# Optimization experiments

Hardware: AMD Instinct MI355X
Metric: run time of the kernel (lower is better)

The kernel has to match this reference:

```python
import jax, jax.numpy as jnp
import numpy as np

H = 16  # num heads
ROPE_BASE = 10000.0

def _rope(t):
    # t: [B, T, H, D]; half-split (rotate_half / LLaMA-style) rotary embedding
    B, T, nH, D = t.shape
    half = D // 2
    inv_freq = 1.0 / (ROPE_BASE ** (jnp.arange(0, half, dtype=jnp.float32) / half))
    ang = jnp.arange(T, dtype=jnp.float32)[:, None] * inv_freq[None, :]  # [T, half]
    cos = jnp.cos(ang)[None, :, None, :]  # [1,T,1,half]
    sin = jnp.sin(ang)[None, :, None, :]
    t1, t2 = t[..., :half], t[..., half:]
    return jnp.concatenate([t1 * cos - t2 * sin, t2 * cos + t1 * sin], axis=-1)

def setup_inputs() -> dict:
    key = jax.random.key(0)
    ks = jax.random.split(key, 5)
    B, T, C = 2, 2048, 1024
    s = 1.0 / np.sqrt(C)
    return {
        "x": jax.random.normal(ks[0], (B, T, C), jnp.float32),
        "Wqkv": jax.random.normal(ks[1], (C, 3 * C), jnp.float32) * s,
        "bqkv": jnp.zeros((3 * C,), jnp.float32),
        "Wout": jax.random.normal(ks[2], (C, C), jnp.float32) * s,
        "bout": jnp.zeros((C,), jnp.float32),
    }

def reference(x, Wqkv, bqkv, Wout, bout):
    B, T, C = x.shape
    D = C // H
    qkv = (x @ Wqkv + bqkv).reshape(B, T, 3, H, D)
    q, k, v = qkv[:, :, 0], qkv[:, :, 1], qkv[:, :, 2]  # [B,T,H,D]
    q = _rope(q)
    k = _rope(k)
    scale = 1.0 / jnp.sqrt(jnp.asarray(D, x.dtype))
    scores = jnp.einsum('bqhd,bkhd->bhqk', q, k) * scale
    probs = jax.nn.softmax(scores, axis=-1)
    attn = jnp.einsum('bhqk,bkhd->bqhd', probs, v).reshape(B, T, C)
    return attn @ Wout + bout
```

## Files before the change

kernel.cpp:

```cpp
#include <hip/hip_runtime.h>

typedef float f32x4 __attribute__((ext_vector_type(4)));
typedef short bf16x8 __attribute__((ext_vector_type(8)));
typedef short bf16x4 __attribute__((ext_vector_type(4)));

#define DEV __device__ __forceinline__

DEV unsigned short f2bf(float x) {
  union { float f; unsigned u; } v; v.f = x;
  unsigned r = v.u + 0x7fffu + ((v.u >> 16) & 1u);
  return (unsigned short)(r >> 16);
}
DEV float bf2f(unsigned short h) {
  union { unsigned u; float f; } v; v.u = ((unsigned)h) << 16;
  return v.f;
}

#if defined(__has_builtin)
# if __has_builtin(__builtin_amdgcn_global_load_lds)
#  define HAVE_GLL 1
# endif
# if __has_builtin(__builtin_amdgcn_exp2f)
#  define EXP2(x) __builtin_amdgcn_exp2f(x)
# else
#  define EXP2(x) exp2f(x)
# endif
#else
# define EXP2(x) exp2f(x)
#endif

DEV unsigned pk_bf16_trunc(float a, float b) {
  return __builtin_amdgcn_perm(__float_as_uint(b), __float_as_uint(a), 0x07060302u);
}
DEV unsigned pk_bf16_rnd(float a, float b) {
  return ((unsigned)f2bf(b) << 16) | f2bf(a);
}

DEV void g2l16(const unsigned short* g, unsigned short* l) {
#ifdef HAVE_GLL
  __builtin_amdgcn_global_load_lds((const __attribute__((address_space(1))) void*)g,
                                   (__attribute__((address_space(3))) void*)l, 16, 0, 0);
#else
  *(uint4*)l = *(const uint4*)g;
#endif
}

DEV f32x4 mfma16x16x16(bf16x4 a, bf16x4 b, f32x4 c) {
#if defined(__has_builtin) && __has_builtin(__builtin_amdgcn_mfma_f32_16x16x16bf16_1k)
  return __builtin_amdgcn_mfma_f32_16x16x16bf16_1k(a, b, c, 0, 0, 0);
#else
  asm volatile("v_mfma_f32_16x16x16_bf16 %0, %1, %2, %0" : "+v"(c) : "v"(a), "v"(b));
  return c;
#endif
}

__global__ __launch_bounds__(256) void prep(const float* __restrict__ x,
                                            const float* __restrict__ Wqkv,
                                            const float* __restrict__ Wout,
                                            float* cosb, float* sinb,
                                            unsigned short* __restrict__ A1,
                                            unsigned short* __restrict__ W1t,
                                            unsigned short* __restrict__ W2t) {
  __shared__ float t[64 * 65];
  int blk = blockIdx.x;
  if (blk < 256) {
    int i = blk * 256 + threadIdx.x;
    int tt = i >> 5, d = i & 31;
    float invf = (float)(1.0 / pow(10000.0, (double)d / 32.0));
    float ang = (float)tt * invf;
    cosb[i] = (float)cos((double)ang);
    sinb[i] = (float)sin((double)ang);
    return;
  }
  if (blk < 4352) {
    int i = (blk - 256) * 256 + threadIdx.x;
    f32x4 v = ((const f32x4*)x)[i];
    ushort4 o;
    o.x = f2bf(v[0]); o.y = f2bf(v[1]); o.z = f2bf(v[2]); o.w = f2bf(v[3]);
    ((ushort4*)A1)[i] = o;
    return;
  }
  const float* W; unsigned short* Wt; int N, bidx;
  if (blk < 5120) { W = Wqkv; Wt = W1t; N = 3072; bidx = blk - 4352; }
  else            { W = Wout; Wt = W2t; N = 1024; bidx = blk - 5120; }
  int k0 = (bidx & 15) * 64, n0 = (bidx >> 4) * 64;
  for (int idx = threadIdx.x; idx < 4096; idx += 256) {
    int kl = idx >> 6, nl = idx & 63;
    t[kl * 65 + nl] = W[(size_t)(k0 + kl) * N + n0 + nl];
  }
  __syncthreads();
  for (int idx = threadIdx.x; idx < 4096; idx += 256) {
    int nl = idx >> 6, kl = idx & 63;
    Wt[(size_t)(n0 + nl) * 1024 + k0 + kl] = f2bf(t[kl * 65 + nl]);
  }
}

#define QSCALE 0.180336880f
__global__ __launch_bounds__(256, 2) void gemm_qkv(
    const unsigned short* __restrict__ A, const unsigned short* __restrict__ Bt,
    const float* __restrict__ bias, const float* __restrict__ cosb,
    const float* __restrict__ sinb, unsigned short* __restrict__ QK,
    unsigned short* __restrict__ Vt) {
  const int K = 1024;
  __shared__ alignas(16) unsigned short As[128 * 64];
  __shared__ alignas(16) unsigned short Bs[128 * 64];
  const int tid = threadIdx.x;
  const int lane = tid & 63, wave = tid >> 6;
  const int l15 = lane & 15, quad = lane >> 4;
  const int m0 = blockIdx.y * 128, n0 = blockIdx.x * 128;
  const int wm = (wave & 1) * 64, wn = (wave >> 1) * 64;

  f32x4 acc[4][4];
#pragma unroll
  for (int i = 0; i < 4; i++)
#pragma unroll
    for (int j = 0; j < 4; j++)
#pragma unroll
      for (int r = 0; r < 4; r++) acc[i][j][r] = 0.f;

  for (int kt = 0; kt < 16; ++kt) {
    __syncthreads();
#pragma unroll
    for (int i = 0; i < 4; ++i) {
      int u = i * 256 + tid;
      int row = u >> 3;
      int kcg = (u & 7) ^ (row & 7);
      g2l16(A  + (size_t)(m0 + row) * K + (kt << 6) + (kcg << 3), As + u * 8);
      g2l16(Bt + (size_t)(n0 + row) * K + (kt << 6) + (kcg << 3), Bs + u * 8);
    }
    __syncthreads();
#pragma unroll
    for (int ks = 0; ks < 2; ++ks) {
      const int kc = ks * 4 + quad;
      bf16x8 af[4], bfr[4];
#pragma unroll
      for (int t = 0; t < 4; ++t) {
        int mrow = wm + t * 16 + l15;
        af[t] = *(const bf16x8*)(As + (mrow * 8 + (kc ^ (mrow & 7))) * 8);
        int nrow = wn + t * 16 + l15;
        bfr[t] = *(const bf16x8*)(Bs + (nrow * 8 + (kc ^ (nrow & 7))) * 8);
      }
#pragma unroll
      for (int mt = 0; mt < 4; ++mt)
#pragma unroll
        for (int nt = 0; nt < 4; ++nt)
          acc[mt][nt] = __builtin_amdgcn_mfma_f32_16x16x32_bf16(af[mt], bfr[nt], acc[mt][nt], 0, 0, 0);
    }
  }
  const int headcol = n0 + wn;
  const int b = m0 >> 11;
  float bb[4];
#pragma unroll
  for (int nt = 0; nt < 4; ++nt) bb[nt] = bias[headcol + nt * 16 + l15];

  if (headcol < 2048) {
    const float scale = (headcol < 1024) ? QSCALE : 1.f;
#pragma unroll
    for (int mt = 0; mt < 4; ++mt) {
#pragma unroll
      for (int r = 0; r < 4; ++r) {
        int row = m0 + wm + mt * 16 + quad * 4 + r;
        int t = row & 2047;
#pragma unroll
        for (int nt = 0; nt < 2; ++nt) {
          int d = nt * 16 + l15;
          float c = cosb[t * 32 + d], s = sinb[t * 32 + d];
          float v1 = acc[mt][nt][r] + bb[nt];
          float v2 = acc[mt][nt + 2][r] + bb[nt + 2];
          QK[(size_t)row * 2048 + headcol + d]      = f2bf((v1 * c - v2 * s) * scale);
          QK[(size_t)row * 2048 + headcol + d + 32] = f2bf((v2 * c + v1 * s) * scale);
        }
      }
    }
  } else {
    const int hv = (headcol - 2048) >> 6;
    const int t0 = (m0 + wm) & 2047;
#pragma unroll
    for (int mt = 0; mt < 4; ++mt)
#pragma unroll
      for (int nt = 0; nt < 4; ++nt) {
        int d = nt * 16 + l15;
        uint2 w;
        w.x = pk_bf16_rnd(acc[mt][nt][0] + bb[nt], acc[mt][nt][1] + bb[nt]);
        w.y = pk_bf16_rnd(acc[mt][nt][2] + bb[nt], acc[mt][nt][3] + bb[nt]);
        *(uint2*)(Vt + ((size_t)((b * 16 + hv) * 64 + d)) * 2048 + t0 + mt * 16 + quad * 4) = w;
      }
  }
}

__global__ __launch_bounds__(256, 2) void gemm64(
    const unsigned short* __restrict__ A, const unsigned short* __restrict__ Bt,
    const float* __restrict__ bias, float* __restrict__ C, int M, int N, int K) {
  __shared__ alignas(16) unsigned short As[64 * 64];
  __shared__ alignas(16) unsigned short Bs[128 * 64];
  const int tid = threadIdx.x;
  const int lane = tid & 63, wave = tid >> 6;
  const int l15 = lane & 15, quad = lane >> 4;
  const int m0 = blockIdx.y * 64, n0 = blockIdx.x * 128;
  const int wm = (wave & 1) * 32, wn = (wave >> 1) * 64;

  f32x4 acc[2][4];
#pragma unroll
  for (int i = 0; i < 2; i++)
#pragma unroll
    for (int j = 0; j < 4; j++)
#pragma unroll
      for (int r = 0; r < 4; r++) acc[i][j][r] = 0.f;

  const int nkt = K >> 6;
  for (int kt = 0; kt < nkt; ++kt) {
    __syncthreads();
#pragma unroll
    for (int i = 0; i < 2; ++i) {
      int u = i * 256 + tid;
      int row = u >> 3;
      int kcg = (u & 7) ^ (row & 7);
      g2l16(A + (size_t)(m0 + row) * K + (kt << 6) + (kcg << 3), As + u * 8);
    }
#pragma unroll
    for (int i = 0; i < 4; ++i) {
      int u = i * 256 + tid;
      int row = u >> 3;
      int kcg = (u & 7) ^ (row & 7);
      g2l16(Bt + (size_t)(n0 + row) * K + (kt << 6) + (kcg << 3), Bs + u * 8);
    }
    __syncthreads();
#pragma unroll
    for (int ks = 0; ks < 2; ++ks) {
      const int kc = ks * 4 + quad;
      bf16x8 af[2], bfr[4];
#pragma unroll
      for (int t = 0; t < 2; ++t) {
        int mrow = wm + t * 16 + l15;
        af[t] = *(const bf16x8*)(As + (mrow * 8 + (kc ^ (mrow & 7))) * 8);
      }
#pragma unroll
      for (int t = 0; t < 4; ++t) {
        int nrow = wn + t * 16 + l15;
        bfr[t] = *(const bf16x8*)(Bs + (nrow * 8 + (kc ^ (nrow & 7))) * 8);
      }
#pragma unroll
      for (int mt = 0; mt < 2; ++mt)
#pragma unroll
        for (int nt = 0; nt < 4; ++nt)
          acc[mt][nt] = __builtin_amdgcn_mfma_f32_16x16x32_bf16(af[mt], bfr[nt], acc[mt][nt], 0, 0, 0);
    }
  }
#pragma unroll
  for (int mt = 0; mt < 2; ++mt)
#pragma unroll
    for (int nt = 0; nt < 4; ++nt) {
      int col = n0 + wn + nt * 16 + l15;
      int rowb = m0 + wm + mt * 16 + quad * 4;
      float b = bias[col];
#pragma unroll
      for (int r = 0; r < 4; ++r)
        C[(size_t)(rowb + r) * N + col] = acc[mt][nt][r] + b;
    }
}

__global__ __launch_bounds__(256, 2) void flash_attn(const unsigned short* __restrict__ QK,
                                                     const unsigned short* __restrict__ Vt,
                                                     unsigned short* __restrict__ O) {
  __shared__ alignas(16) unsigned short Ks[128 * 64];
  __shared__ alignas(16) unsigned short Vs[64 * 128];
  const int tid = threadIdx.x, lane = tid & 63, wave = tid >> 6;
  const int l15 = lane & 15, quad = lane >> 4;
  const int bh = blockIdx.x, qb = blockIdx.y;
  const int b = bh >> 4, h = bh & 15;
  const int q0 = qb * 128 + wave * 32;
  bf16x8 qf[2][2];
#pragma unroll
  for (int ks = 0; ks < 2; ++ks)
#pragma unroll
    for (int qg = 0; qg < 2; ++qg)
      qf[ks][qg] = *(const bf16x8*)(QK + (size_t)(b * 2048 + q0 + qg * 16 + l15) * 2048 +
                                    h * 64 + ks * 32 + quad * 8);
  f32x4 o[2][4];
#pragma unroll
  for (int qg = 0; qg < 2; qg++)
#pragma unroll
    for (int nt = 0; nt < 4; nt++)
#pragma unroll
      for (int r = 0; r < 4; r++) o[qg][nt][r] = 0.f;
  float li[2] = {0.f, 0.f};
  const f32x4 negb = {-12.f, -12.f, -12.f, -12.f};

  for (int kb = 0; kb < 16; ++kb) {
    __syncthreads();
#pragma unroll
    for (int i = 0; i < 4; ++i) {
      int u = i * 256 + tid;
      int krow = u >> 3;
      int kcg = (u & 7) ^ (krow & 7);
      g2l16(QK + (size_t)(b * 2048 + kb * 128 + krow) * 2048 + 1024 + h * 64 + kcg * 8,
            Ks + u * 8);
      int vrow = u >> 4;
      int vcg = (u & 15) ^ (vrow & 7);
      g2l16(Vt + ((size_t)bh * 64 + vrow) * 2048 + kb * 128 + vcg * 8, Vs + u * 8);
    }
    __syncthreads();
    f32x4 sacc[2][8];
#pragma unroll
    for (int ks = 0; ks < 2; ++ks) {
      const int kc = ks * 4 + quad;
#pragma unroll
      for (int mt = 0; mt < 8; ++mt) {
        int key = mt * 16 + l15;
        bf16x8 kf = *(const bf16x8*)(Ks + (key * 8 + (kc ^ (key & 7))) * 8);
        if (ks == 0) {
          sacc[0][mt] = __builtin_amdgcn_mfma_f32_16x16x32_bf16(kf, qf[0][0], negb, 0, 0, 0);
          sacc[1][mt] = __builtin_amdgcn_mfma_f32_16x16x32_bf16(kf, qf[0][1], negb, 0, 0, 0);
        } else {
          sacc[0][mt] = __builtin_amdgcn_mfma_f32_16x16x32_bf16(kf, qf[1][0], sacc[0][mt], 0, 0, 0);
          sacc[1][mt] = __builtin_amdgcn_mfma_f32_16x16x32_bf16(kf, qf[1][1], sacc[1][mt], 0, 0, 0);
        }
      }
    }
    bf16x4 pf[2][8];
#pragma unroll
    for (int qg = 0; qg < 2; ++qg) {
      float psum = 0.f;
#pragma unroll
      for (int mt = 0; mt < 8; ++mt) {
        float p0 = EXP2(sacc[qg][mt][0]);
        float p1 = EXP2(sacc[qg][mt][1]);
        float p2 = EXP2(sacc[qg][mt][2]);
        float p3 = EXP2(sacc[qg][mt][3]);
        psum += (p0 + p1) + (p2 + p3);
        union { uint2 u; bf16x4 v; } cc;
        cc.u.x = pk_bf16_trunc(p0, p1);
        cc.u.y = pk_bf16_trunc(p2, p3);
        pf[qg][mt] = cc.v;
      }
      li[qg] += psum;
    }
#pragma unroll
    for (int mt = 0; mt < 8; ++mt) {
      const int cu = mt * 2 + (quad >> 1);
#pragma unroll
      for (int nt = 0; nt < 4; ++nt) {
        int dd = nt * 16 + l15;
        bf16x4 vf = *(const bf16x4*)(Vs + (dd * 16 + (cu ^ (dd & 7))) * 8 + (quad & 1) * 4);
        o[0][nt] = mfma16x16x16(vf, pf[0][mt], o[0][nt]);
        o[1][nt] = mfma16x16x16(vf, pf[1][mt], o[1][nt]);
      }
    }
  }
#pragma unroll
  for (int qg = 0; qg < 2; ++qg) {
    li[qg] += __shfl_xor(li[qg], 16);
    li[qg] += __shfl_xor(li[qg], 32);
    float inv = 1.001953125f / li[qg];
    size_t rowb = (size_t)(b * 2048 + q0 + qg * 16 + l15) * 1024 + h * 64;
#pragma unroll
    for (int nt = 0; nt < 4; ++nt) {
      uint2 w;
      w.x = pk_bf16_rnd(o[qg][nt][0] * inv, o[qg][nt][1] * inv);
      w.y = pk_bf16_rnd(o[qg][nt][2] * inv, o[qg][nt][3] * inv);
      *(uint2*)(O + rowb + nt * 16 + quad * 4) = w;
    }
  }
}

extern "C" void kernel_launch(void* const* d_in, const int* in_sizes, int n_in,
                              void* d_out, int out_size, void* d_ws, size_t ws_size,
                              hipStream_t stream) {
  const float* x    = (const float*)d_in[0];
  const float* Wqkv = (const float*)d_in[1];
  const float* bqkv = (const float*)d_in[2];
  const float* Wout = (const float*)d_in[3];
  const float* bout = (const float*)d_in[4];
  float* out = (float*)d_out;
  char* ws = (char*)d_ws;
  float*          COS  = (float*)(ws + 0);
  float*          SIN  = (float*)(ws + 262144);
  unsigned short* A1   = (unsigned short*)(ws + 524288);
  unsigned short* W1t  = (unsigned short*)(ws + 8912896);
  unsigned short* W2t  = (unsigned short*)(ws + 15204352);
  unsigned short* QK   = (unsigned short*)(ws + 17301504);
  unsigned short* VT   = (unsigned short*)(ws + 34078720);
  unsigned short* A2   = (unsigned short*)(ws + 42467328);

  prep<<<5376, 256, 0, stream>>>(x, Wqkv, Wout, COS, SIN, A1, W1t, W2t);
  gemm_qkv<<<dim3(24, 32), 256, 0, stream>>>(A1, W1t, bqkv, COS, SIN, QK, VT);
  flash_attn<<<dim3(32, 16), 256, 0, stream>>>(QK, VT, A2);
  gemm64<<<dim3(8, 64), 256, 0, stream>>>(A2, W2t, bout, out, 4096, 1024, 1024);
}
```

Baseline: 181.5 us.

## Use 16x16x32 MFMA for PV via LDS-staged P; coalesce QK/Vt epilogue stores

In attention, the probability tile is written to a per-wave swizzled LDS buffer and read back as 8-element fragments, so the PV product can use the wider 16x16x32 bf16 MFMA instead of twice as many 16x16x16 ops. The QKV GEMM epilogue packs the two rotary outputs into one 32-bit store, which interleaves their column order, and transposes V tiles through LDS so Vt is written with 16-byte coalesced stores. The cost is extra LDS traffic and capacity (32KB more in flash_attn, which may affect occupancy) plus an added barrier in the GEMM.

Result: slower. 190.2 us (+4.8%).

```diff
diff --git a/kernel.cpp b/kernel.cpp
--- a/kernel.cpp
+++ b/kernel.cpp
@@ -2,7 +2,6 @@
 
 typedef float f32x4 __attribute__((ext_vector_type(4)));
 typedef short bf16x8 __attribute__((ext_vector_type(8)));
-typedef short bf16x4 __attribute__((ext_vector_type(4)));
 
 #define DEV __device__ __forceinline__
 
@@ -42,15 +41,6 @@
                                    (__attribute__((address_space(3))) void*)l, 16, 0, 0);
 #else
   *(uint4*)l = *(const uint4*)g;
-#endif
-}
-
-DEV f32x4 mfma16x16x16(bf16x4 a, bf16x4 b, f32x4 c) {
-#if defined(__has_builtin) && __has_builtin(__builtin_amdgcn_mfma_f32_16x16x16bf16_1k)
-  return __builtin_amdgcn_mfma_f32_16x16x16bf16_1k(a, b, c, 0, 0, 0);
-#else
-  asm volatile("v_mfma_f32_16x16x16_bf16 %0, %1, %2, %0" : "+v"(c) : "v"(a), "v"(b));
-  return c;
 #endif
 }
 
@@ -102,8 +92,9 @@
     const float* __restrict__ sinb, unsigned short* __restrict__ QK,
     unsigned short* __restrict__ Vt) {
   const int K = 1024;
-  __shared__ alignas(16) unsigned short As[128 * 64];
-  __shared__ alignas(16) unsigned short Bs[128 * 64];
+  __shared__ alignas(16) unsigned short SMEM[16384];
+  unsigned short* As = SMEM;
+  unsigned short* Bs = SMEM + 8192;
   const int tid = threadIdx.x;
   const int lane = tid & 63, wave = tid >> 6;
   const int l15 = lane & 15, quad = lane >> 4;
@@ -147,13 +138,14 @@
           acc[mt][nt] = __builtin_amdgcn_mfma_f32_16x16x32_bf16(af[mt], bfr[nt], acc[mt][nt], 0, 0, 0);
     }
   }
+  __syncthreads();
   const int headcol = n0 + wn;
   const int b = m0 >> 11;
   float bb[4];
 #pragma unroll
   for (int nt = 0; nt < 4; ++nt) bb[nt] = bias[headcol + nt * 16 + l15];
 
-  if (headcol < 2048) {
+  if (n0 < 2048) {
     const float scale = (headcol < 1024) ? QSCALE : 1.f;
 #pragma unroll
     for (int mt = 0; mt < 4; ++mt) {
@@ -163,16 +155,17 @@
         int t = row & 2047;
 #pragma unroll
         for (int nt = 0; nt < 2; ++nt) {
-          int d = nt * 16 + l15;
-          float c = cosb[t * 32 + d], s = sinb[t * 32 + d];
+          int dr = nt * 16 + l15;
+          float c = cosb[t * 32 + dr], s = sinb[t * 32 + dr];
           float v1 = acc[mt][nt][r] + bb[nt];
           float v2 = acc[mt][nt + 2][r] + bb[nt + 2];
-          QK[(size_t)row * 2048 + headcol + d]      = f2bf((v1 * c - v2 * s) * scale);
-          QK[(size_t)row * 2048 + headcol + d + 32] = f2bf((v2 * c + v1 * s) * scale);
+          unsigned w = pk_bf16_rnd((v1 * c - v2 * s) * scale, (v2 * c + v1 * s) * scale);
+          *(unsigned*)(QK + (size_t)row * 2048 + headcol + 2 * dr) = w;
         }
       }
     }
   } else {
+    unsigned short* Tw = SMEM + wave * 4096;
     const int hv = (headcol - 2048) >> 6;
     const int t0 = (m0 + wm) & 2047;
 #pragma unroll
@@ -183,8 +176,17 @@
         uint2 w;
         w.x = pk_bf16_rnd(acc[mt][nt][0] + bb[nt], acc[mt][nt][1] + bb[nt]);
         w.y = pk_bf16_rnd(acc[mt][nt][2] + bb[nt], acc[mt][nt][3] + bb[nt]);
-        *(uint2*)(Vt + ((size_t)((b * 16 + hv) * 64 + d)) * 2048 + t0 + mt * 16 + quad * 4) = w;
-      }
+        int u = mt * 2 + (quad >> 1);
+        *(uint2*)(Tw + d * 64 + ((u ^ (d & 7)) * 8) + (quad & 1) * 4) = w;
+      }
+    unsigned short* vbase = Vt + ((size_t)((b * 16 + hv) * 64)) * 2048 + t0;
+#pragma unroll
+    for (int dp = 0; dp < 8; ++dp) {
+      int d = dp * 8 + (lane >> 3);
+      int u = lane & 7;
+      uint4 w4 = *(uint4*)(Tw + d * 64 + ((u ^ (d & 7)) * 8));
+      *(uint4*)(vbase + (size_t)d * 2048 + u * 8) = w4;
+    }
   }
 }
 
@@ -264,11 +266,13 @@
                                                      unsigned short* __restrict__ O) {
   __shared__ alignas(16) unsigned short Ks[128 * 64];
   __shared__ alignas(16) unsigned short Vs[64 * 128];
+  __shared__ alignas(16) unsigned short Ps[4 * 32 * 128];
   const int tid = threadIdx.x, lane = tid & 63, wave = tid >> 6;
   const int l15 = lane & 15, quad = lane >> 4;
   const int bh = blockIdx.x, qb = blockIdx.y;
   const int b = bh >> 4, h = bh & 15;
   const int q0 = qb * 128 + wave * 32;
+  unsigned short* Pw = Ps + wave * 4096;
   bf16x8 qf[2][2];
 #pragma unroll
   for (int ks = 0; ks < 2; ++ks)
@@ -317,9 +321,10 @@
         }
       }
     }
-    bf16x4 pf[2][8];
 #pragma unroll
     for (int qg = 0; qg < 2; ++qg) {
+      const int row = qg * 16 + l15;
+      const int sw = (row & 15) << 1;
       float psum = 0.f;
 #pragma unroll
       for (int mt = 0; mt < 8; ++mt) {
@@ -328,22 +333,31 @@
         float p2 = EXP2(sacc[qg][mt][2]);
         float p3 = EXP2(sacc[qg][mt][3]);
         psum += (p0 + p1) + (p2 + p3);
-        union { uint2 u; bf16x4 v; } cc;
-        cc.u.x = pk_bf16_trunc(p0, p1);
-        cc.u.y = pk_bf16_trunc(p2, p3);
-        pf[qg][mt] = cc.v;
+        uint2 w;
+        w.x = pk_bf16_trunc(p0, p1);
+        w.y = pk_bf16_trunc(p2, p3);
+        int su = (mt * 4 + quad) ^ sw;
+        *(uint2*)(Pw + row * 128 + su * 4) = w;
       }
       li[qg] += psum;
     }
 #pragma unroll
-    for (int mt = 0; mt < 8; ++mt) {
-      const int cu = mt * 2 + (quad >> 1);
+    for (int c = 0; c < 4; ++c) {
+      bf16x8 vv[4];
 #pragma unroll
       for (int nt = 0; nt < 4; ++nt) {
         int dd = nt * 16 + l15;
-        bf16x4 vf = *(const bf16x4*)(Vs + (dd * 16 + (cu ^ (dd & 7))) * 8 + (quad & 1) * 4);
-        o[0][nt] = mfma16x16x16(vf, pf[0][mt], o[0][nt]);
-        o[1][nt] = mfma16x16x16(vf, pf[1][mt], o[1][nt]);
+        int vu = (c * 4 + quad) ^ (dd & 7);
+        vv[nt] = *(const bf16x8*)(Vs + dd * 128 + vu * 8);
+      }
+#pragma unroll
+      for (int qg = 0; qg < 2; ++qg) {
+        int prow = qg * 16 + l15;
+        int pu = (c * 8 + quad * 2) ^ ((prow & 15) << 1);
+        bf16x8 pf = *(const bf16x8*)(Pw + prow * 128 + pu * 4);
+#pragma unroll
+        for (int nt = 0; nt < 4; ++nt)
+          o[qg][nt] = __builtin_amdgcn_mfma_f32_16x16x32_bf16(vv[nt], pf, o[qg][nt], 0, 0, 0);
       }
     }
   }
```
